# Optimization experiments

Measured on AMD Instinct MI355X. Metric: run time of the kernel, lower is better.

Reference implementation:

```python
import jax, jax.numpy as jnp
import numpy as np


def setup_inputs() -> dict:
    key = jax.random.key(0)
    k1, k2, k3, k4 = jax.random.split(key, 4)
    B, L, T = 8, 2048, 1024
    Dh, Dg, Dp = 1024, 768, 256
    H = jax.random.normal(k1, (B, L, Dh), dtype=jnp.float32)
    G = jax.random.normal(k2, (B, T, Dg), dtype=jnp.float32)
    # nn.Linear(d_g, d_proj, bias=False).weight -> [d_proj, d_g]
    Wq = jax.random.normal(k3, (Dp, Dg), dtype=jnp.float32) * (Dg ** -0.5)
    Wk = jax.random.normal(k4, (Dp, Dh), dtype=jnp.float32) * (Dh ** -0.5)
    return {"H": H, "G": G, "Wq": Wq, "Wk": Wk}


def reference(H, G, Wq, Wk):
    # GO-token queries attend over protein residues; values are the raw H.
    # The torch module computes this with streaming chunks + online LSE,
    # which is mathematically identical to a single stable softmax attention.
    d_proj = Wq.shape[0]
    scale = d_proj ** -0.5
    Q = jnp.einsum('btg,pg->btp', G, Wq)          # [B,T,Dp]
    K = jnp.einsum('blh,ph->blp', H, Wk)          # [B,L,Dp]
    logits = jnp.einsum('btp,blp->btl', Q, K) * scale  # [B,T,L] fp32
    alpha = jax.nn.softmax(logits, axis=-1)
    # denominator clamp matches torch's s.clamp_min(1e-20) (no-op for unmasked)
    Z = jnp.einsum('btl,blh->bth', alpha, H)      # [B,T,Dh]
    return Z
```

## Files before the change

### kernel.cpp

```cpp
#include <hip/hip_runtime.h>
#include <hip/hip_bf16.h>
#include <type_traits>


typedef float    f32x4  __attribute__((ext_vector_type(4)));
typedef __bf16   bf16x8 __attribute__((ext_vector_type(8)));
typedef unsigned short u16x8 __attribute__((ext_vector_type(8)));

__device__ __forceinline__ unsigned short f2bf(float f) {
    union { __bf16 b; unsigned short u; } c;
    c.b = (__bf16)f;
    return c.u;
}
__device__ __forceinline__ float bf2f(unsigned short u) {
    union { unsigned u; float f; } x; x.u = ((unsigned)u) << 16;
    return x.f;
}
__device__ __forceinline__ void gload_lds16(const unsigned short* g, unsigned short* l) {
    __builtin_amdgcn_global_load_lds(
        (const __attribute__((address_space(1))) void*)g,
        (__attribute__((address_space(3))) void*)l, 16, 0, 0);
}

__global__ __launch_bounds__(256) void kn_transp(const float* __restrict__ H,
                                                 unsigned short* __restrict__ HT,
                                                 unsigned short* __restrict__ Hbf,
                                                 const float* __restrict__ Wq,
                                                 const float* __restrict__ Wk,
                                                 unsigned short* __restrict__ Wqbf,
                                                 unsigned short* __restrict__ Wkbf,
                                                 float* __restrict__ rowsum,
                                                 int L, int D, int nq8, int nk8, int nrs4) {
    __shared__ float tile[64][65];
    int b = blockIdx.z;
    const float* src = H + (size_t)b * L * D;
    unsigned short* dstT = HT + (size_t)b * L * D;
    unsigned short* dstN = Hbf + (size_t)b * L * D;
    int l0 = blockIdx.y * 64, d0 = blockIdx.x * 64;
    int rh = threadIdx.x >> 3;
    int c8 = (threadIdx.x & 7) * 8;

    int fid = blockIdx.x + gridDim.x * (blockIdx.y + gridDim.y * blockIdx.z);
    if (fid == 0) {
        f32x4 z = {};
        for (int j = threadIdx.x; j < nrs4; j += 256)
            *(f32x4*)(rowsum + (size_t)j * 4) = z;
    }
    {
        int i = fid * 256 + threadIdx.x;
        if (i < nq8 + nk8) {
            const float* s;
            unsigned short* dp;
            int idx;
            if (i < nq8) { idx = i; s = Wq; dp = Wqbf; }
            else         { idx = i - nq8; s = Wk; dp = Wkbf; }
            f32x4 a = *(const f32x4*)(s + (size_t)idx * 8);
            f32x4 bb = *(const f32x4*)(s + (size_t)idx * 8 + 4);
            u16x8 o;
#pragma unroll
            for (int j = 0; j < 4; ++j) { o[j] = f2bf(a[j]); o[4 + j] = f2bf(bb[j]); }
            *(u16x8*)(dp + (size_t)idx * 8) = o;
        }
    }

#pragma unroll
    for (int i = 0; i < 2; ++i) {
        int r = rh + i * 32;
        const float* p = &src[(size_t)(l0 + r) * D + d0 + c8];
        f32x4 v0 = *(const f32x4*)p;
        f32x4 v1 = *(const f32x4*)(p + 4);
        u16x8 o;
#pragma unroll
        for (int j = 0; j < 4; ++j) {
            o[j] = f2bf(v0[j]); o[4 + j] = f2bf(v1[j]);
            tile[r][c8 + j] = v0[j];
            tile[r][c8 + 4 + j] = v1[j];
        }
        *(u16x8*)&dstN[(size_t)(l0 + r) * D + d0 + c8] = o;
    }
    __syncthreads();
#pragma unroll
    for (int i = 0; i < 2; ++i) {
        int d = rh + i * 32;
        u16x8 o;
#pragma unroll
        for (int j = 0; j < 8; ++j) o[j] = f2bf(tile[c8 + j][d]);
        *(u16x8*)&dstT[(size_t)(d0 + d) * L + l0 + c8] = o;
    }
}

__device__ __forceinline__ void qproj_body(char* smem_raw,
                                           const float* __restrict__ A,
                                           const unsigned short* __restrict__ B,
                                           unsigned short* __restrict__ C,
                                           int N, int K, int t) {
    unsigned short* sA = (unsigned short*)smem_raw;
    unsigned short* sB = sA + 32 * 64;
    float* st = (float*)smem_raw;

    int tid = threadIdx.x;
    int by = t >> 1;
    int bx = t & 1;
    const float* Ab = A + (size_t)by * 32 * K;
    const unsigned short* Bb = B + (size_t)bx * 128 * K;

    int lane = tid & 63;
    int wid = tid >> 6;
    int lr = lane & 15;
    int lg = lane >> 4;
    int xoff = (lane & 7) << 3;

    f32x4 acc[2][2] = {};

    for (int k0 = 0; k0 < K; k0 += 64) {
#pragma unroll
        for (int c = 0; c < 4; ++c) {
            int ch = c * 256 + tid;
            int row = ch >> 3;
            int g8 = (ch & 7) ^ (row & 7);
            gload_lds16(Bb + (size_t)row * K + k0 + g8 * 8, sB + ch * 8);
        }
        {
            int ch = tid;
            int row = ch >> 3;
            const float* srcp = Ab + (size_t)row * K + k0 + (ch & 7) * 8;
            f32x4 v0 = *(const f32x4*)srcp;
            f32x4 v1 = *(const f32x4*)(srcp + 4);
            u16x8 o;
#pragma unroll
            for (int j = 0; j < 4; ++j) { o[j] = f2bf(v0[j]); o[4 + j] = f2bf(v1[j]); }
            int sl = (ch & 7) ^ (row & 7);
            *(u16x8*)&sA[row * 64 + sl * 8] = o;
        }
        __syncthreads();
#pragma unroll
        for (int kk = 0; kk < 2; ++kk) {
            int kb = (kk * 32 + lg * 8) ^ xoff;
            bf16x8 af[2], bfr[2];
#pragma unroll
            for (int m = 0; m < 2; ++m)
                af[m] = *(const bf16x8*)&sA[(m * 16 + lr) * 64 + kb];
#pragma unroll
            for (int n = 0; n < 2; ++n)
                bfr[n] = *(const bf16x8*)&sB[(wid * 32 + n * 16 + lr) * 64 + kb];
#pragma unroll
            for (int m = 0; m < 2; ++m)
#pragma unroll
                for (int n = 0; n < 2; ++n)
                    acc[m][n] = __builtin_amdgcn_mfma_f32_16x16x32_bf16(af[m], bfr[n], acc[m][n], 0, 0, 0);
        }
        __syncthreads();
    }

#pragma unroll
    for (int m = 0; m < 2; ++m) {
        int r0 = m * 16 + lg * 4;
#pragma unroll
        for (int n = 0; n < 2; ++n) {
            int c0 = wid * 32 + n * 16 + lr;
#pragma unroll
            for (int j = 0; j < 4; ++j)
                st[(r0 + j) * 132 + c0] = acc[m][n][j];
        }
    }
    __syncthreads();
    int r  = tid >> 3;
    int c0 = (tid & 7) * 16;
    size_t grow = (size_t)(by * 32 + r) * N + bx * 128 + c0;
#pragma unroll
    for (int g = 0; g < 2; ++g) {
        f32x4 a = *(const f32x4*)&st[r * 132 + c0 + g * 8];
        f32x4 b = *(const f32x4*)&st[r * 132 + c0 + g * 8 + 4];
        u16x8 o;
#pragma unroll
        for (int j = 0; j < 4; ++j) { o[j] = f2bf(a[j]); o[4 + j] = f2bf(b[j]); }
        *(u16x8*)&C[grow + g * 8] = o;
    }
}

__device__ __forceinline__ void kproj_body(char* smem_raw,
                                           const unsigned short* __restrict__ A,
                                           const unsigned short* __restrict__ B,
                                           unsigned short* __restrict__ C,
                                           int N, int K, int t) {
    unsigned short* sA = (unsigned short*)smem_raw;
    unsigned short* sB = sA + 64 * 64;
    float* st = (float*)smem_raw;

    int tid = threadIdx.x;
    int by = t >> 1;
    int bx = t & 1;
    const unsigned short* Ab = A + (size_t)by * 64 * K;
    const unsigned short* Bb = B + (size_t)bx * 128 * K;

    int lane = tid & 63;
    int wid = tid >> 6;
    int wr = wid >> 1, wc = wid & 1;
    int lr = lane & 15;
    int lg = lane >> 4;
    int xoff = (lane & 7) << 3;

    f32x4 acc[2][4] = {};

    for (int k0 = 0; k0 < K; k0 += 64) {
#pragma unroll
        for (int c = 0; c < 2; ++c) {
            int ch = c * 256 + tid;
            int row = ch >> 3;
            int g8 = (ch & 7) ^ (row & 7);
            gload_lds16(Ab + (size_t)row * K + k0 + g8 * 8, sA + ch * 8);
        }
#pragma unroll
        for (int c = 0; c < 4; ++c) {
            int ch = c * 256 + tid;
            int row = ch >> 3;
            int g8 = (ch & 7) ^ (row & 7);
            gload_lds16(Bb + (size_t)row * K + k0 + g8 * 8, sB + ch * 8);
        }
        __syncthreads();
#pragma unroll
        for (int kk = 0; kk < 2; ++kk) {
            int kb = (kk * 32 + lg * 8) ^ xoff;
            bf16x8 af[2], bfr[4];
#pragma unroll
            for (int m = 0; m < 2; ++m)
                af[m] = *(const bf16x8*)&sA[(wr * 32 + m * 16 + lr) * 64 + kb];
#pragma unroll
            for (int n = 0; n < 4; ++n)
                bfr[n] = *(const bf16x8*)&sB[(wc * 64 + n * 16 + lr) * 64 + kb];
#pragma unroll
            for (int m = 0; m < 2; ++m)
#pragma unroll
                for (int n = 0; n < 4; ++n)
                    acc[m][n] = __builtin_amdgcn_mfma_f32_16x16x32_bf16(af[m], bfr[n], acc[m][n], 0, 0, 0);
        }
        __syncthreads();
    }

#pragma unroll
    for (int m = 0; m < 2; ++m) {
        int r0 = wr * 32 + m * 16 + lg * 4;
#pragma unroll
        for (int n = 0; n < 4; ++n) {
            int c0 = wc * 64 + n * 16 + lr;
#pragma unroll
            for (int j = 0; j < 4; ++j)
                st[(r0 + j) * 132 + c0] = acc[m][n][j];
        }
    }
    __syncthreads();
    int r  = tid >> 2;
    int c0 = (tid & 3) * 32;
    size_t grow = (size_t)(by * 64 + r) * N + bx * 128 + c0;
#pragma unroll
    for (int g = 0; g < 4; ++g) {
        f32x4 a = *(const f32x4*)&st[r * 132 + c0 + g * 8];
        f32x4 b = *(const f32x4*)&st[r * 132 + c0 + g * 8 + 4];
        u16x8 o;
#pragma unroll
        for (int j = 0; j < 4; ++j) { o[j] = f2bf(a[j]); o[4 + j] = f2bf(b[j]); }
        *(u16x8*)&C[grow + g * 8] = o;
    }
}

__global__ __launch_bounds__(256) void kn_proj(const unsigned short* __restrict__ Hbf,
                                               const unsigned short* __restrict__ Wkbf,
                                               unsigned short* __restrict__ Kbf,
                                               const float* __restrict__ G,
                                               const unsigned short* __restrict__ Wqbf,
                                               unsigned short* __restrict__ Qbf,
                                               int Dp, int Dh, int Dg) {
    __shared__ __align__(16) char smem_raw[64 * 132 * 4];
    int wg = blockIdx.x;
    if (wg < 512) kproj_body(smem_raw, Hbf, Wkbf, Kbf, Dp, Dh, wg);
    else          qproj_body(smem_raw, G, Wqbf, Qbf, Dp, Dg, wg - 512);
}

__global__ __launch_bounds__(512) void kn_sgemm(const unsigned short* __restrict__ A,
                                                const unsigned short* __restrict__ B,
                                                unsigned short* __restrict__ C,
                                                float* __restrict__ rowsum,
                                                int N, int K, int Trows,
                                                long batchA, long batchB, long batchC,
                                                float scale, int gxs) {
    __shared__ __align__(16) char smem_raw[49152];
    unsigned short* base = (unsigned short*)smem_raw;
    float* st = (float*)smem_raw;

    int tid = threadIdx.x;
    int wg = blockIdx.x;
    int bz = wg & 7;
    int t = wg >> 3;
    int by = t >> gxs;
    int bx = t & ((1 << gxs) - 1);

    const unsigned short* Ab = A + (size_t)bz * batchA + (size_t)by * 256 * K;
    const unsigned short* Bb = B + (size_t)bz * batchB + (size_t)bx * 128 * K;
    unsigned short* Cb = C + (size_t)bz * batchC;
    float* rs = rowsum + (size_t)bz * Trows;

    int lane = tid & 63;
    int wid = tid >> 6;
    int wr = wid >> 1, wc = wid & 1;
    int lr = lane & 15;
    int lg = lane >> 4;
    int xoff = (lane & 7) << 3;

    f32x4 acc[4][4] = {};

    for (int k0 = 0; k0 < K; k0 += 64) {
#pragma unroll
        for (int c = 0; c < 6; ++c) {
            int ch = c * 512 + tid;
            if (ch < 2048) {
                int row = ch >> 3;
                int g8 = (ch & 7) ^ (row & 7);
                gload_lds16(Ab + (size_t)row * K + k0 + g8 * 8, base + ch * 8);
            } else {
                int bc = ch - 2048;
                int row = bc >> 3;
                int g8 = (bc & 7) ^ (row & 7);
                gload_lds16(Bb + (size_t)row * K + k0 + g8 * 8, base + 16384 + bc * 8);
            }
        }
        __syncthreads();
#pragma unroll
        for (int kk = 0; kk < 2; ++kk) {
            int kb = (kk * 32 + lg * 8) ^ xoff;
            bf16x8 af[4], bfr[4];
#pragma unroll
            for (int m = 0; m < 4; ++m)
                af[m] = *(const bf16x8*)&base[(wr * 64 + m * 16 + lr) * 64 + kb];
#pragma unroll
            for (int n = 0; n < 4; ++n)
                bfr[n] = *(const bf16x8*)&base[16384 + (wc * 64 + n * 16 + lr) * 64 + kb];
#pragma unroll
            for (int m = 0; m < 4; ++m)
#pragma unroll
                for (int n = 0; n < 4; ++n)
                    acc[m][n] = __builtin_amdgcn_mfma_f32_16x16x32_bf16(af[m], bfr[n], acc[m][n], 0, 0, 0);
        }
        __syncthreads();
    }

#pragma unroll
    for (int q = 0; q < 4; ++q) {
        if (wr == q) {
#pragma unroll
            for (int m = 0; m < 4; ++m) {
                int rl = m * 16 + lg * 4;
#pragma unroll
                for (int n = 0; n < 4; ++n) {
                    int col = wc * 64 + n * 16 + lr;
#pragma unroll
                    for (int j = 0; j < 4; ++j)
                        st[(rl + j) * 132 + col] = acc[m][n][j] * scale;
                }
            }
        }
        __syncthreads();
        int r = tid >> 3;
        int c0 = (tid & 7) * 16;
        int grow_r = by * 256 + q * 64 + r;
        size_t grow = (size_t)grow_r * N + bx * 128 + c0;
        float psum = 0.f;
#pragma unroll
        for (int g = 0; g < 2; ++g) {
            f32x4 a = *(const f32x4*)&st[r * 132 + c0 + g * 8];
            f32x4 b = *(const f32x4*)&st[r * 132 + c0 + g * 8 + 4];
            u16x8 o;
#pragma unroll
            for (int j = 0; j < 4; ++j) {
                o[j]     = f2bf(__expf(a[j]));
                o[4 + j] = f2bf(__expf(b[j]));
                psum += bf2f(o[j]) + bf2f(o[4 + j]);
            }
            *(u16x8*)&Cb[grow + g * 8] = o;
        }
        psum += __shfl_xor(psum, 1);
        psum += __shfl_xor(psum, 2);
        psum += __shfl_xor(psum, 4);
        if ((tid & 7) == 0)
            atomicAdd(&rs[grow_r], psum);
        __syncthreads();
    }
}

__global__ __launch_bounds__(512) void kn_pv(const unsigned short* __restrict__ A,
                                             const unsigned short* __restrict__ B,
                                             float* __restrict__ C,
                                             const float* __restrict__ rowsum,
                                             int N, int K, int Trows,
                                             long batchA, long batchB, long batchC,
                                             int gxs) {
    __shared__ __align__(16) char smem_raw[2 * 49152];
    unsigned short* base = (unsigned short*)smem_raw;
    float* st = (float*)smem_raw;

    int tid = threadIdx.x;
    int wg = blockIdx.x;
    int bz = wg & 7;
    int t = wg >> 3;
    int by = t >> gxs;
    int bx = t & ((1 << gxs) - 1);

    const unsigned short* Ab = A + (size_t)bz * batchA + (size_t)by * 256 * K;
    const unsigned short* Bb = B + (size_t)bz * batchB + (size_t)bx * 128 * K;
    float* Cb = C + (size_t)bz * batchC;
    const float* rs = rowsum + (size_t)bz * Trows;

    int lane = tid & 63;
    int wid = tid >> 6;
    int wr = wid >> 1, wc = wid & 1;
    int lr = lane & 15;
    int lg = lane >> 4;
    int xoff = (lane & 7) << 3;

    f32x4 acc[4][4] = {};

    auto STAGE = [&](int buf, int k0) {
        unsigned short* dA = base + buf * 24576;
        unsigned short* dB = dA + 16384;
#pragma unroll
        for (int c = 0; c < 6; ++c) {
            int ch = c * 512 + tid;
            if (ch < 2048) {
                int row = ch >> 3;
                int g8 = (ch & 7) ^ (row & 7);
                gload_lds16(Ab + (size_t)row * K + k0 + g8 * 8, dA + ch * 8);
            } else {
                int bc = ch - 2048;
                int row = bc >> 3;
                int g8 = (bc & 7) ^ (row & 7);
                gload_lds16(Bb + (size_t)row * K + k0 + g8 * 8, dB + bc * 8);
            }
        }
    };
    auto COMPUTE = [&](int buf) {
        unsigned short* pA = base + buf * 24576;
        unsigned short* pB = pA + 16384;
#pragma unroll
        for (int kk = 0; kk < 2; ++kk) {
            int kb = (kk * 32 + lg * 8) ^ xoff;
            bf16x8 af[4], bfr[4];
#pragma unroll
            for (int m = 0; m < 4; ++m)
                af[m] = *(const bf16x8*)&pA[(wr * 64 + m * 16 + lr) * 64 + kb];
#pragma unroll
            for (int n = 0; n < 4; ++n)
                bfr[n] = *(const bf16x8*)&pB[(wc * 64 + n * 16 + lr) * 64 + kb];
#pragma unroll
            for (int m = 0; m < 4; ++m)
#pragma unroll
                for (int n = 0; n < 4; ++n)
                    acc[m][n] = __builtin_amdgcn_mfma_f32_16x16x32_bf16(af[m], bfr[n], acc[m][n], 0, 0, 0);
        }
    };

    int nt = K / 64;
    STAGE(0, 0);
    __syncthreads();
    int cur = 0;
    for (int tt = 0; tt < nt; ++tt) {
        if (tt + 1 < nt) STAGE(cur ^ 1, (tt + 1) * 64);
        COMPUTE(cur);
        __syncthreads();
        cur ^= 1;
    }

#pragma unroll
    for (int q = 0; q < 4; ++q) {
        if (wr == q) {
#pragma unroll
            for (int m = 0; m < 4; ++m) {
                int rl = m * 16 + lg * 4;
#pragma unroll
                for (int n = 0; n < 4; ++n) {
                    int col = wc * 64 + n * 16 + lr;
#pragma unroll
                    for (int j = 0; j < 4; ++j)
                        st[(rl + j) * 132 + col] = acc[m][n][j];
                }
            }
        }
        __syncthreads();
        int r = tid >> 3;
        int c0 = (tid & 7) * 16;
        float inv = 1.0f / rs[by * 256 + q * 64 + r];
        size_t grow = (size_t)(by * 256 + q * 64 + r) * N + bx * 128 + c0;
#pragma unroll
        for (int g = 0; g < 4; ++g) {
            f32x4 v = *(const f32x4*)&st[r * 132 + c0 + g * 4];
#pragma unroll
            for (int j = 0; j < 4; ++j) v[j] *= inv;
            *(f32x4*)&Cb[grow + g * 4] = v;
        }
        __syncthreads();
    }
}

extern "C" void kernel_launch(void* const* d_in, const int* in_sizes, int n_in,
                              void* d_out, int out_size, void* d_ws, size_t ws_size,
                              hipStream_t stream) {
    constexpr int B = 8, L = 2048, T = 1024, Dh = 1024, Dg = 768, Dp = 256;
    const float* H  = (const float*)d_in[0];
    const float* G  = (const float*)d_in[1];
    const float* Wq = (const float*)d_in[2];
    const float* Wk = (const float*)d_in[3];
    float* Z = (float*)d_out;

    unsigned short* Qbf  = (unsigned short*)d_ws;
    unsigned short* Kbf  = Qbf + (size_t)B * T * Dp;
    unsigned short* HT   = Kbf + (size_t)B * L * Dp;
    unsigned short* S    = HT  + (size_t)B * Dh * L;
    unsigned short* Hbf  = S   + (size_t)B * T * L;
    unsigned short* Wqbf = Hbf + (size_t)B * L * Dh;
    unsigned short* Wkbf = Wqbf + (size_t)Dp * Dg;
    float* rowsum = (float*)(Wkbf + (size_t)Dp * Dh);

    int nq8 = Dp * Dg / 8, nk8 = Dp * Dh / 8;

    kn_transp<<<dim3(Dh / 64, L / 64, B), dim3(256), 0, stream>>>
        (H, HT, Hbf, Wq, Wk, Wqbf, Wkbf, rowsum, L, Dh, nq8, nk8, B * T / 4);

    kn_proj<<<1024, 256, 0, stream>>>(Hbf, Wkbf, Kbf, G, Wqbf, Qbf, Dp, Dh, Dg);

    kn_sgemm<<<(T / 256) * (L / 128) * B, 512, 0, stream>>>
        (Qbf, Kbf, S, rowsum, L, Dp, T, (long)T * Dp, (long)L * Dp, (long)T * L, 0.0625f, 4);

    kn_pv<<<(T / 256) * (Dh / 128) * B, 512, 0, stream>>>
        (S, HT, Z, rowsum, Dh, L, T, (long)T * L, (long)Dh * L, (long)T * Dh, 3);
}
```

Baseline: 119.3 us.

## Double-buffer LDS in score GEMM and shrink tile to 128x128 with 256 threads

The QK^T score kernel now prefetches the next K-slice into a second LDS buffer while the current one is computed. It also drops the block tile from 256x128 with 512 threads to 128x128 with 256 threads, doubling the grid. The epilogue is re-indexed for 64-row halves, with a 4-lane row-sum reduction before the atomic add. The aim is to hide global-to-LDS latency and improve occupancy and load balance. The cost is twice the LDS per block, and the reduction dimension is only four 64-wide steps, so there is little loop to pipeline.

```diff
diff --git a/kernel.cpp b/kernel.cpp
--- a/kernel.cpp
+++ b/kernel.cpp
@@ -276,14 +276,14 @@
     else          qproj_body(smem_raw, G, Wqbf, Qbf, Dp, Dg, wg - 512);
 }
 
-__global__ __launch_bounds__(512) void kn_sgemm(const unsigned short* __restrict__ A,
-                                                const unsigned short* __restrict__ B,
-                                                unsigned short* __restrict__ C,
-                                                float* __restrict__ rowsum,
-                                                int N, int K, int Trows,
-                                                long batchA, long batchB, long batchC,
-                                                float scale, int gxs) {
-    __shared__ __align__(16) char smem_raw[49152];
+__global__ __launch_bounds__(256) void kn_sgemm(const unsigned short* __restrict__ A,
+                                               const unsigned short* __restrict__ B,
+                                               unsigned short* __restrict__ C,
+                                               float* __restrict__ rowsum,
+                                               int N, int K, int Trows,
+                                               long batchA, long batchB, long batchC,
+                                               float scale, int gxs) {
+    __shared__ __align__(16) char smem_raw[2 * 32768];
     unsigned short* base = (unsigned short*)smem_raw;
     float* st = (float*)smem_raw;
 
@@ -294,7 +294,7 @@
     int by = t >> gxs;
     int bx = t & ((1 << gxs) - 1);
 
-    const unsigned short* Ab = A + (size_t)bz * batchA + (size_t)by * 256 * K;
+    const unsigned short* Ab = A + (size_t)bz * batchA + (size_t)by * 128 * K;
     const unsigned short* Bb = B + (size_t)bz * batchB + (size_t)bx * 128 * K;
     unsigned short* Cb = C + (size_t)bz * batchC;
     float* rs = rowsum + (size_t)bz * Trows;
@@ -308,44 +308,53 @@
 
     f32x4 acc[4][4] = {};
 
-    for (int k0 = 0; k0 < K; k0 += 64) {
-#pragma unroll
-        for (int c = 0; c < 6; ++c) {
-            int ch = c * 512 + tid;
-            if (ch < 2048) {
-                int row = ch >> 3;
-                int g8 = (ch & 7) ^ (row & 7);
-                gload_lds16(Ab + (size_t)row * K + k0 + g8 * 8, base + ch * 8);
-            } else {
-                int bc = ch - 2048;
-                int row = bc >> 3;
-                int g8 = (bc & 7) ^ (row & 7);
-                gload_lds16(Bb + (size_t)row * K + k0 + g8 * 8, base + 16384 + bc * 8);
-            }
-        }
-        __syncthreads();
+    auto STAGE = [&](int buf, int k0) {
+        unsigned short* dA = base + buf * 16384;
+        unsigned short* dB = dA + 8192;
+#pragma unroll
+        for (int c = 0; c < 8; ++c) {
+            int ch = (c & 3) * 256 + tid;
+            int row = ch >> 3;
+            int g8 = (ch & 7) ^ (row & 7);
+            if (c < 4) gload_lds16(Ab + (size_t)row * K + k0 + g8 * 8, dA + ch * 8);
+            else       gload_lds16(Bb + (size_t)row * K + k0 + g8 * 8, dB + ch * 8);
+        }
+    };
+    auto COMPUTE = [&](int buf) {
+        unsigned short* pA = base + buf * 16384;
+        unsigned short* pB = pA + 8192;
 #pragma unroll
         for (int kk = 0; kk < 2; ++kk) {
             int kb = (kk * 32 + lg * 8) ^ xoff;
             bf16x8 af[4], bfr[4];
 #pragma unroll
             for (int m = 0; m < 4; ++m)
-                af[m] = *(const bf16x8*)&base[(wr * 64 + m * 16 + lr) * 64 + kb];
+                af[m] = *(const bf16x8*)&pA[(wr * 64 + m * 16 + lr) * 64 + kb];
 #pragma unroll
             for (int n = 0; n < 4; ++n)
-                bfr[n] = *(const bf16x8*)&base[16384 + (wc * 64 + n * 16 + lr) * 64 + kb];
+                bfr[n] = *(const bf16x8*)&pB[(wc * 64 + n * 16 + lr) * 64 + kb];
 #pragma unroll
             for (int m = 0; m < 4; ++m)
 #pragma unroll
                 for (int n = 0; n < 4; ++n)
                     acc[m][n] = __builtin_amdgcn_mfma_f32_16x16x32_bf16(af[m], bfr[n], acc[m][n], 0, 0, 0);
         }
-        __syncthreads();
-    }
-
-#pragma unroll
-    for (int q = 0; q < 4; ++q) {
-        if (wr == q) {
+    };
+
+    int nt = K / 64;
+    STAGE(0, 0);
+    __syncthreads();
+    int cur = 0;
+    for (int tt = 0; tt < nt; ++tt) {
+        if (tt + 1 < nt) STAGE(cur ^ 1, (tt + 1) * 64);
+        COMPUTE(cur);
+        __syncthreads();
+        cur ^= 1;
+    }
+
+#pragma unroll
+    for (int half = 0; half < 2; ++half) {
+        if (wr == half) {
 #pragma unroll
             for (int m = 0; m < 4; ++m) {
                 int rl = m * 16 + lg * 4;
@@ -359,13 +368,13 @@
             }
         }
         __syncthreads();
-        int r = tid >> 3;
-        int c0 = (tid & 7) * 16;
-        int grow_r = by * 256 + q * 64 + r;
+        int r = tid >> 2;
+        int c0 = (tid & 3) * 32;
+        int grow_r = by * 128 + half * 64 + r;
         size_t grow = (size_t)grow_r * N + bx * 128 + c0;
         float psum = 0.f;
 #pragma unroll
-        for (int g = 0; g < 2; ++g) {
+        for (int g = 0; g < 4; ++g) {
             f32x4 a = *(const f32x4*)&st[r * 132 + c0 + g * 8];
             f32x4 b = *(const f32x4*)&st[r * 132 + c0 + g * 8 + 4];
             u16x8 o;
@@ -379,8 +388,7 @@
         }
         psum += __shfl_xor(psum, 1);
         psum += __shfl_xor(psum, 2);
-        psum += __shfl_xor(psum, 4);
-        if ((tid & 7) == 0)
+        if ((tid & 3) == 0)
             atomicAdd(&rs[grow_r], psum);
         __syncthreads();
     }
@@ -525,7 +533,7 @@
 
     kn_proj<<<1024, 256, 0, stream>>>(Hbf, Wkbf, Kbf, G, Wqbf, Qbf, Dp, Dh, Dg);
 
-    kn_sgemm<<<(T / 256) * (L / 128) * B, 512, 0, stream>>>
+    kn_sgemm<<<(T / 128) * (L / 128) * B, 256, 0, stream>>>
         (Qbf, Kbf, S, rowsum, L, Dp, T, (long)T * Dp, (long)L * Dp, (long)T * L, 0.0625f, 4);
 
     kn_pv<<<(T / 256) * (Dh / 128) * B, 512, 0, stream>>>
```

Result: slower. 123.8 us (+3.7%).
